# Performance work log

Hardware: AMD Instinct MI355X
Metric: run time of the kernel (lower is better)

The kernel has to match this reference:

```python
import jax, jax.numpy as jnp
import numpy as np

B, L, D = 4096, 200, 64
N_ITEMS, N_USERS, N_RATINGS = 100000, 100000, 5


def setup_inputs() -> dict:
    key = jax.random.key(0)
    ks = jax.random.split(key, 10)
    nodes = jax.random.randint(ks[0], (B,), 0, N_USERS)
    history_uv = jax.random.randint(ks[1], (B, L), 0, N_ITEMS)
    history_r = jax.random.randint(ks[2], (B, L), 0, N_RATINGS)
    s = 1.0 / np.sqrt(D)
    v2e = jax.random.normal(ks[3], (N_ITEMS, D), dtype=jnp.float32)
    r2e = jax.random.normal(ks[4], (N_RATINGS, D), dtype=jnp.float32)
    # torch Linear: weight is [out, in]
    w1_W = jax.random.uniform(ks[5], (D, 2 * D), dtype=jnp.float32, minval=-s, maxval=s)
    w1_b = jax.random.uniform(ks[6], (D,), dtype=jnp.float32, minval=-s, maxval=s)
    w2_W = jax.random.uniform(ks[7], (D, D), dtype=jnp.float32, minval=-s, maxval=s)
    w2_b = jax.random.uniform(ks[8], (D,), dtype=jnp.float32, minval=-s, maxval=s)
    return {
        "v2e": v2e, "r2e": r2e,
        "w1_W": w1_W, "w1_b": w1_b, "w2_W": w2_W, "w2_b": w2_b,
        "nodes": nodes, "history_uv": history_uv, "history_r": history_r,
    }


def reference(v2e, r2e, w1_W, w1_b, w2_W, w2_b, nodes, history_uv, history_r):
    # Gather item and rating embeddings for every (node, history slot): [B, L, D]
    e_uv = v2e[history_uv]
    e_r = r2e[history_r]
    # concat -> [B, L, 2D], two-layer MLP with ReLU
    x = jnp.concatenate([e_uv, e_r], axis=-1)
    h = jax.nn.relu(jnp.einsum("bli,oi->blo", x, w1_W) + w1_b)
    o = jax.nn.relu(jnp.einsum("bli,oi->blo", h, w2_W) + w2_b)
    # uv=True branch: plain mean over the history dimension (nodes/u2e unused)
    return jnp.mean(o, axis=1)  # [B, D]
```

## Files before the change

kernel.cpp:

```cpp
#include <hip/hip_runtime.h>

#define NITEMS 100000
#define NRATE  5
#define BB     4096
#define LL     200
#define DD     64
#define NTILES 6250
#define NWAVES 3128
#define NW_REM 3122

typedef short short8  __attribute__((ext_vector_type(8)));
typedef float f32x4   __attribute__((ext_vector_type(4)));
typedef float f32x2   __attribute__((ext_vector_type(2)));
typedef int   i32x4   __attribute__((ext_vector_type(4)));

static __device__ __forceinline__ short f2bf(float f) {
  return (short)((__builtin_bit_cast(unsigned, f) + 0x8000u) >> 16);
}
static __device__ __forceinline__ unsigned pk2bf(float a, float b) {
  const unsigned ua = __builtin_bit_cast(unsigned, a) + 0x8000u;
  const unsigned ub = __builtin_bit_cast(unsigned, b) + 0x8000u;
  return __builtin_amdgcn_perm(ub, ua, 0x07060302u);
}
static __device__ __forceinline__ int kperm(int p) {
  return ((p & 3) << 4) | (p >> 2);
}

#if __has_builtin(__builtin_elementwise_max)
static __device__ __forceinline__ f32x2 relu2(f32x2 v) {
  return __builtin_elementwise_max(v, f32x2{0.f, 0.f});
}
static __device__ __forceinline__ f32x4 relu4(f32x4 v) {
  return __builtin_elementwise_max(v, f32x4{0.f, 0.f, 0.f, 0.f});
}
#else
static __device__ __forceinline__ f32x2 relu2(f32x2 v) {
  return f32x2{fmaxf(v.x, 0.f), fmaxf(v.y, 0.f)};
}
static __device__ __forceinline__ f32x4 relu4(f32x4 v) {
  return f32x4{fmaxf(v[0], 0.f), fmaxf(v[1], 0.f), fmaxf(v[2], 0.f), fmaxf(v[3], 0.f)};
}
#endif

__global__ __launch_bounds__(256) void k_pre(
    const float* __restrict__ v2e, const float* __restrict__ r2e,
    const float* __restrict__ w1W, const float* __restrict__ w1b,
    const float* __restrict__ w2W,
    unsigned char* __restrict__ pre8, short* __restrict__ w2p,
    float* __restrict__ r5p)
{
  const int tid = threadIdx.x;
  const int blk = blockIdx.x;

  if (blk == 0) {
    for (int idx = tid; idx < 64 * 64; idx += 256) {
      const int o = idx >> 6, p = idx & 63;
      w2p[idx] = f2bf(w2W[o * 64 + kperm(p)]);
    }
    for (int idx = tid; idx < NRATE * 64; idx += 256) {
      const int r = idx >> 6, p = idx & 63;
      const int o = kperm(p);
      const float4* wr = reinterpret_cast<const float4*>(w1W + o * 128 + 64);
      const float4* rr = reinterpret_cast<const float4*>(r2e + r * 64);
      float s = w1b[o];
#pragma unroll
      for (int q = 0; q < 16; ++q) {
        const float4 a = wr[q], b = rr[q];
        s += a.x * b.x + a.y * b.y + a.z * b.z + a.w * b.w;
      }
      r5p[r * 64 + p] = s;
    }
    return;
  }

  const int wave = tid >> 6, lane = tid & 63;
  const int n = lane & 15, quad = lane >> 4;
  const int gw = (blk - 1) * 4 + wave;
  const int ntile = (gw < NW_REM) ? 2 : 1;

  const int q0 = ((n >> 1) & 3) * 16 + (n >> 3) * 8 + (n & 1) * 4;

  int tile = gw;
  float4 cur0, cur1, cur2, cur3;
  {
    const size_t row = (size_t)(tile * 16 + n);
    const float4* p = reinterpret_cast<const float4*>(v2e + row * 64 + quad * 8);
    cur0 = p[0]; cur1 = p[1];
    const float4* q = reinterpret_cast<const float4*>(v2e + row * 64 + 32 + quad * 8);
    cur2 = q[0]; cur3 = q[1];
  }

  short8 bfr[2][4];
#pragma unroll
  for (int nt = 0; nt < 4; ++nt)
#pragma unroll
    for (int kh = 0; kh < 2; ++kh) {
      const float4* p = reinterpret_cast<const float4*>(
          w1W + (nt * 16 + n) * 128 + kh * 32 + quad * 8);
      const float4 x0 = p[0], x1 = p[1];
      i32x4 pk = {(int)pk2bf(x0.x, x0.y), (int)pk2bf(x0.z, x0.w),
                  (int)pk2bf(x1.x, x1.y), (int)pk2bf(x1.z, x1.w)};
      bfr[kh][nt] = __builtin_bit_cast(short8, pk);
    }

  for (int it = 0; it < ntile; ++it) {
    const int next = tile + NWAVES;
    float4 nx0, nx1, nx2, nx3;
    if (it + 1 < ntile) {
      const size_t row = (size_t)(next * 16 + n);
      const float4* p = reinterpret_cast<const float4*>(v2e + row * 64 + quad * 8);
      nx0 = p[0]; nx1 = p[1];
      const float4* q = reinterpret_cast<const float4*>(v2e + row * 64 + 32 + quad * 8);
      nx2 = q[0]; nx3 = q[1];
    }

    short8 afr[2];
    {
      i32x4 pk0 = {(int)pk2bf(cur0.x, cur0.y), (int)pk2bf(cur0.z, cur0.w),
                   (int)pk2bf(cur1.x, cur1.y), (int)pk2bf(cur1.z, cur1.w)};
      afr[0] = __builtin_bit_cast(short8, pk0);
      i32x4 pk1 = {(int)pk2bf(cur2.x, cur2.y), (int)pk2bf(cur2.z, cur2.w),
                   (int)pk2bf(cur3.x, cur3.y), (int)pk2bf(cur3.z, cur3.w)};
      afr[1] = __builtin_bit_cast(short8, pk1);
    }

    f32x4 d[4];
#pragma unroll
    for (int nt = 0; nt < 4; ++nt) {
      f32x4 z = {0.f, 0.f, 0.f, 0.f};
      z = __builtin_amdgcn_mfma_f32_16x16x32_bf16(afr[0], bfr[0][nt], z, 0, 0, 0);
      z = __builtin_amdgcn_mfma_f32_16x16x32_bf16(afr[1], bfr[1][nt], z, 0, 0, 0);
      d[nt] = z;
    }

    const int ib = tile * 16;
#pragma unroll
    for (int r = 0; r < 4; ++r) {
      const int item = ib + quad * 4 + r;
      int pkd = 0;
      pkd = __builtin_amdgcn_cvt_pk_fp8_f32(d[0][r], d[1][r], pkd, false);
      pkd = __builtin_amdgcn_cvt_pk_fp8_f32(d[2][r], d[3][r], pkd, true);
      *reinterpret_cast<int*>(pre8 + (size_t)item * 64 + q0) = pkd;
    }

    tile = next;
    cur0 = nx0; cur1 = nx1; cur2 = nx2; cur3 = nx3;
  }
}

__global__ __launch_bounds__(256) void k_main(
    const unsigned char* __restrict__ pre8, const float* __restrict__ r5p,
    const short* __restrict__ w2p, const float* __restrict__ w2b,
    const int* __restrict__ huv, const int* __restrict__ hrr,
    float* __restrict__ out)
{
  __shared__ __align__(16) float s_r5[4][5 * 68];

  const int tid  = threadIdx.x;
  const int wave = tid >> 6, lane = tid & 63;
  const int n = lane & 15, quad = lane >> 4;
  const int b = blockIdx.x * 4 + wave;

  const int* hu = huv + b * LL;
  const int* hr = hrr + b * LL;

  int iv[13], ir[13];
#pragma unroll
  for (int t = 0; t < 12; ++t) {
    iv[t] = hu[t * 16 + n];
    ir[t] = hr[t * 16 + n];
  }
  {
    const int lc = min(192 + n, LL - 1);
    iv[12] = hu[lc];
    ir[12] = hr[lc];
  }

  i32x4 g[13];
#pragma unroll
  for (int t = 0; t < 13; ++t)
    g[t] = *reinterpret_cast<const i32x4*>(
        pre8 + (size_t)iv[t] * 64 + quad * 16);

#pragma unroll
  for (int i = 0; i < 5; ++i) {
    const int idx = i * 64 + lane;
    s_r5[wave][(idx >> 6) * 68 + (idx & 63)] = r5p[idx];
  }

  short8 bfr[2][4];
#pragma unroll
  for (int nt = 0; nt < 4; ++nt)
#pragma unroll
    for (int kh = 0; kh < 2; ++kh)
      bfr[kh][nt] = *reinterpret_cast<const short8*>(
          w2p + (nt * 16 + n) * 64 + kh * 32 + quad * 8);

  f32x4 zb[4];
#pragma unroll
  for (int nt = 0; nt < 4; ++nt) {
    const float bv = w2b[nt * 16 + n];
    zb[nt] = f32x4{bv, bv, bv, bv};
  }

  const float tailm = (quad < 2) ? 1.0f : 0.0f;
  f32x4 acc4[4] = {{0.f,0.f,0.f,0.f},{0.f,0.f,0.f,0.f},
                   {0.f,0.f,0.f,0.f},{0.f,0.f,0.f,0.f}};

#pragma unroll
  for (int t = 0; t < 13; ++t) {
    const float* rbase = &s_r5[wave][ir[t] * 68 + quad * 8];
    const f32x4 ra = *reinterpret_cast<const f32x4*>(rbase);
    const f32x4 rb = *reinterpret_cast<const f32x4*>(rbase + 4);
    const f32x4 rc = *reinterpret_cast<const f32x4*>(rbase + 32);
    const f32x4 rd = *reinterpret_cast<const f32x4*>(rbase + 36);

    short8 afr[2];
    {
      f32x2 p0 = relu2(__builtin_amdgcn_cvt_pk_f32_fp8(g[t][0], false) + f32x2{ra[0], ra[1]});
      f32x2 p1 = relu2(__builtin_amdgcn_cvt_pk_f32_fp8(g[t][0], true)  + f32x2{ra[2], ra[3]});
      f32x2 p2 = relu2(__builtin_amdgcn_cvt_pk_f32_fp8(g[t][1], false) + f32x2{rb[0], rb[1]});
      f32x2 p3 = relu2(__builtin_amdgcn_cvt_pk_f32_fp8(g[t][1], true)  + f32x2{rb[2], rb[3]});
      i32x4 hpk = {(int)pk2bf(p0.x, p0.y), (int)pk2bf(p1.x, p1.y),
                   (int)pk2bf(p2.x, p2.y), (int)pk2bf(p3.x, p3.y)};
      afr[0] = __builtin_bit_cast(short8, hpk);
    }
    {
      f32x2 p0 = relu2(__builtin_amdgcn_cvt_pk_f32_fp8(g[t][2], false) + f32x2{rc[0], rc[1]});
      f32x2 p1 = relu2(__builtin_amdgcn_cvt_pk_f32_fp8(g[t][2], true)  + f32x2{rc[2], rc[3]});
      f32x2 p2 = relu2(__builtin_amdgcn_cvt_pk_f32_fp8(g[t][3], false) + f32x2{rd[0], rd[1]});
      f32x2 p3 = relu2(__builtin_amdgcn_cvt_pk_f32_fp8(g[t][3], true)  + f32x2{rd[2], rd[3]});
      i32x4 hpk = {(int)pk2bf(p0.x, p0.y), (int)pk2bf(p1.x, p1.y),
                   (int)pk2bf(p2.x, p2.y), (int)pk2bf(p3.x, p3.y)};
      afr[1] = __builtin_bit_cast(short8, hpk);
    }

    __builtin_amdgcn_s_setprio(1);
    f32x4 d[4];
#pragma unroll
    for (int nt = 0; nt < 4; ++nt) {
      f32x4 z = zb[nt];
      z = __builtin_amdgcn_mfma_f32_16x16x32_bf16(afr[0], bfr[0][nt], z, 0, 0, 0);
      z = __builtin_amdgcn_mfma_f32_16x16x32_bf16(afr[1], bfr[1][nt], z, 0, 0, 0);
      d[nt] = z;
    }
    __builtin_amdgcn_s_setprio(0);

#pragma unroll
    for (int nt = 0; nt < 4; ++nt) {
      f32x4 mx = relu4(d[nt]);
      if (t == 12) mx = mx * tailm;
      acc4[nt] += mx;
    }
  }

  float acc[4];
#pragma unroll
  for (int nt = 0; nt < 4; ++nt) {
    float v = (acc4[nt][0] + acc4[nt][1]) + (acc4[nt][2] + acc4[nt][3]);
    v += __shfl_xor(v, 16, 64);
    v += __shfl_xor(v, 32, 64);
    acc[nt] = v;
  }

  out[b * 64 + quad * 16 + n] = acc[quad] * (1.0f / (float)LL);
}

__global__ __launch_bounds__(256) void k_fallback(
    const float* __restrict__ v2e, const float* __restrict__ r2e,
    const float* __restrict__ w1W, const float* __restrict__ w1b,
    const float* __restrict__ w2W, const float* __restrict__ w2b,
    const int* __restrict__ huv, const int* __restrict__ hrr,
    float* __restrict__ out)
{
  __shared__ float sw1[64][129];
  __shared__ float sw2[64][65];
  __shared__ float sx[4][128];
  __shared__ float sh[4][64];
  __shared__ float red[4][64];

  const int tid = threadIdx.x;
  const int wave = tid >> 6, lane = tid & 63;
  const int b = blockIdx.x;

  for (int idx = tid; idx < 64 * 128; idx += 256) sw1[idx >> 7][idx & 127] = w1W[idx];
  for (int idx = tid; idx < 64 * 64; idx += 256) sw2[idx >> 6][idx & 63] = w2W[idx];
  __syncthreads();

  const float b1o = w1b[lane], b2o = w2b[lane];
  float acc = 0.f;

  for (int l = wave; l < LL; l += 4) {
    const int iv = huv[b * LL + l];
    const int ir = hrr[b * LL + l];
    sx[wave][lane]      = v2e[iv * 64 + lane];
    sx[wave][64 + lane] = r2e[ir * 64 + lane];
    __syncthreads();
    float h = b1o;
    for (int i = 0; i < 128; ++i) h += sx[wave][i] * sw1[lane][i];
    sh[wave][lane] = fmaxf(h, 0.f);
    __syncthreads();
    float o = b2o;
    for (int i = 0; i < 64; ++i) o += sh[wave][i] * sw2[lane][i];
    acc += fmaxf(o, 0.f);
  }

  red[wave][lane] = acc;
  __syncthreads();
  if (tid < 64) {
    const float s = red[0][tid] + red[1][tid] + red[2][tid] + red[3][tid];
    out[b * 64 + tid] = s * (1.0f / (float)LL);
  }
}

extern "C" void kernel_launch(void* const* d_in, const int* in_sizes, int n_in,
                              void* d_out, int out_size, void* d_ws, size_t ws_size,
                              hipStream_t stream) {
  (void)in_sizes; (void)n_in; (void)out_size;
  const float* v2e = (const float*)d_in[0];
  const float* r2e = (const float*)d_in[1];
  const float* w1W = (const float*)d_in[2];
  const float* w1b = (const float*)d_in[3];
  const float* w2W = (const float*)d_in[4];
  const float* w2b = (const float*)d_in[5];
  const int* huv = (const int*)d_in[7];
  const int* hrr = (const int*)d_in[8];
  float* out = (float*)d_out;

  const size_t OFF_R5 = (size_t)NITEMS * 64;
  const size_t OFF_W2 = OFF_R5 + NRATE * 64 * sizeof(float);
  const size_t NEED   = OFF_W2 + 64 * 64 * sizeof(short);

  if (ws_size >= NEED) {
    unsigned char* pre8 = (unsigned char*)d_ws;
    float* r5p = (float*)((char*)d_ws + OFF_R5);
    short* w2p = (short*)((char*)d_ws + OFF_W2);

    k_pre<<<783, 256, 0, stream>>>(v2e, r2e, w1W, w1b, w2W, pre8, w2p, r5p);
    k_main<<<BB / 4, 256, 0, stream>>>(pre8, r5p, w2p, w2b, huv, hrr, out);
  } else {
    k_fallback<<<BB, 256, 0, stream>>>(v2e, r2e, w1W, w1b, w2W, w2b, huv, hrr, out);
  }
}
```

Baseline: 114.1 us.

## Process two batch rows per wave with all gathers issued up front

Each wave now handles two batch rows (b and b+2048). All 26 fp8 embedding-row gathers for both rows are issued before any compute, and the grid is halved to 512 blocks. Rating indices are packed into bytes, four per register, to offset the extra registers needed for the second row's gathered data. The aim is more memory-level parallelism per wave and amortised setup (W2 fragments, bias, rating table). The cost is higher register pressure, which can lower occupancy, and fewer waves overall.

```diff
diff --git a/kernel.cpp b/kernel.cpp
--- a/kernel.cpp
+++ b/kernel.cpp
@@ -148,68 +148,19 @@
   }
 }
 
-__global__ __launch_bounds__(256) void k_main(
-    const unsigned char* __restrict__ pre8, const float* __restrict__ r5p,
-    const short* __restrict__ w2p, const float* __restrict__ w2b,
-    const int* __restrict__ huv, const int* __restrict__ hrr,
-    float* __restrict__ out)
+static __device__ __forceinline__ void tiles_b(
+    const i32x4 (&g)[13], const unsigned (&irp)[4],
+    const float* r5w, const short8 (&bfr)[2][4], const f32x4 (&zb)[4],
+    const int n, const int quad, const float tailm,
+    float* __restrict__ out, const int b)
 {
-  __shared__ __align__(16) float s_r5[4][5 * 68];
-
-  const int tid  = threadIdx.x;
-  const int wave = tid >> 6, lane = tid & 63;
-  const int n = lane & 15, quad = lane >> 4;
-  const int b = blockIdx.x * 4 + wave;
-
-  const int* hu = huv + b * LL;
-  const int* hr = hrr + b * LL;
-
-  int iv[13], ir[13];
-#pragma unroll
-  for (int t = 0; t < 12; ++t) {
-    iv[t] = hu[t * 16 + n];
-    ir[t] = hr[t * 16 + n];
-  }
-  {
-    const int lc = min(192 + n, LL - 1);
-    iv[12] = hu[lc];
-    ir[12] = hr[lc];
-  }
-
-  i32x4 g[13];
-#pragma unroll
-  for (int t = 0; t < 13; ++t)
-    g[t] = *reinterpret_cast<const i32x4*>(
-        pre8 + (size_t)iv[t] * 64 + quad * 16);
-
-#pragma unroll
-  for (int i = 0; i < 5; ++i) {
-    const int idx = i * 64 + lane;
-    s_r5[wave][(idx >> 6) * 68 + (idx & 63)] = r5p[idx];
-  }
-
-  short8 bfr[2][4];
-#pragma unroll
-  for (int nt = 0; nt < 4; ++nt)
-#pragma unroll
-    for (int kh = 0; kh < 2; ++kh)
-      bfr[kh][nt] = *reinterpret_cast<const short8*>(
-          w2p + (nt * 16 + n) * 64 + kh * 32 + quad * 8);
-
-  f32x4 zb[4];
-#pragma unroll
-  for (int nt = 0; nt < 4; ++nt) {
-    const float bv = w2b[nt * 16 + n];
-    zb[nt] = f32x4{bv, bv, bv, bv};
-  }
-
-  const float tailm = (quad < 2) ? 1.0f : 0.0f;
   f32x4 acc4[4] = {{0.f,0.f,0.f,0.f},{0.f,0.f,0.f,0.f},
                    {0.f,0.f,0.f,0.f},{0.f,0.f,0.f,0.f}};
 
 #pragma unroll
   for (int t = 0; t < 13; ++t) {
-    const float* rbase = &s_r5[wave][ir[t] * 68 + quad * 8];
+    const int irt = (int)((irp[t >> 2] >> ((t & 3) * 8)) & 0xFF);
+    const float* rbase = r5w + irt * 68 + quad * 8;
     const f32x4 ra = *reinterpret_cast<const f32x4*>(rbase);
     const f32x4 rb = *reinterpret_cast<const f32x4*>(rbase + 4);
     const f32x4 rc = *reinterpret_cast<const f32x4*>(rbase + 32);
@@ -262,8 +213,84 @@
     v += __shfl_xor(v, 32, 64);
     acc[nt] = v;
   }
-
   out[b * 64 + quad * 16 + n] = acc[quad] * (1.0f / (float)LL);
+}
+
+__global__ __launch_bounds__(256) void k_main(
+    const unsigned char* __restrict__ pre8, const float* __restrict__ r5p,
+    const short* __restrict__ w2p, const float* __restrict__ w2b,
+    const int* __restrict__ huv, const int* __restrict__ hrr,
+    float* __restrict__ out)
+{
+  __shared__ __align__(16) float s_r5[4][5 * 68];
+
+  const int tid  = threadIdx.x;
+  const int wave = tid >> 6, lane = tid & 63;
+  const int n = lane & 15, quad = lane >> 4;
+  const int gw = blockIdx.x * 4 + wave;
+  const int b1 = gw, b2 = gw + 2048;
+
+  int iv1[13], iv2[13];
+  unsigned irp1[4] = {0u,0u,0u,0u}, irp2[4] = {0u,0u,0u,0u};
+  {
+    const int* hu = huv + b1 * LL; const int* hr = hrr + b1 * LL;
+#pragma unroll
+    for (int t = 0; t < 12; ++t) {
+      iv1[t] = hu[t * 16 + n];
+      irp1[t >> 2] |= ((unsigned)hr[t * 16 + n]) << ((t & 3) * 8);
+    }
+    const int lc = min(192 + n, LL - 1);
+    iv1[12] = hu[lc];
+    irp1[3] |= (unsigned)hr[lc];
+  }
+  {
+    const int* hu = huv + b2 * LL; const int* hr = hrr + b2 * LL;
+#pragma unroll
+    for (int t = 0; t < 12; ++t) {
+      iv2[t] = hu[t * 16 + n];
+      irp2[t >> 2] |= ((unsigned)hr[t * 16 + n]) << ((t & 3) * 8);
+    }
+    const int lc = min(192 + n, LL - 1);
+    iv2[12] = hu[lc];
+    irp2[3] |= (unsigned)hr[lc];
+  }
+
+  i32x4 g1[13], g2[13];
+#pragma unroll
+  for (int t = 0; t < 13; ++t)
+    g1[t] = *reinterpret_cast<const i32x4*>(
+        pre8 + (size_t)iv1[t] * 64 + quad * 16);
+#pragma unroll
+  for (int t = 0; t < 13; ++t)
+    g2[t] = *reinterpret_cast<const i32x4*>(
+        pre8 + (size_t)iv2[t] * 64 + quad * 16);
+
+#pragma unroll
+  for (int i = 0; i < 5; ++i) {
+    const int idx = i * 64 + lane;
+    s_r5[wave][(idx >> 6) * 68 + (idx & 63)] = r5p[idx];
+  }
+
+  short8 bfr[2][4];
+#pragma unroll
+  for (int nt = 0; nt < 4; ++nt)
+#pragma unroll
+    for (int kh = 0; kh < 2; ++kh)
+      bfr[kh][nt] = *reinterpret_cast<const short8*>(
+          w2p + (nt * 16 + n) * 64 + kh * 32 + quad * 8);
+
+  f32x4 zb[4];
+#pragma unroll
+  for (int nt = 0; nt < 4; ++nt) {
+    const float bv = w2b[nt * 16 + n];
+    zb[nt] = f32x4{bv, bv, bv, bv};
+  }
+
+  const float tailm = (quad < 2) ? 1.0f : 0.0f;
+  const float* r5w = &s_r5[wave][0];
+
+  tiles_b(g1, irp1, r5w, bfr, zb, n, quad, tailm, out, b1);
+  tiles_b(g2, irp2, r5w, bfr, zb, n, quad, tailm, out, b2);
 }
 
 __global__ __launch_bounds__(256) void k_fallback(
@@ -337,7 +364,7 @@
     short* w2p = (short*)((char*)d_ws + OFF_W2);
 
     k_pre<<<783, 256, 0, stream>>>(v2e, r2e, w1W, w1b, w2W, pre8, w2p, r5p);
-    k_main<<<BB / 4, 256, 0, stream>>>(pre8, r5p, w2p, w2b, huv, hrr, out);
+    k_main<<<512, 256, 0, stream>>>(pre8, r5p, w2p, w2b, huv, hrr, out);
   } else {
     k_fallback<<<BB, 256, 0, stream>>>(v2e, r2e, w1W, w1b, w2W, w2b, huv, hrr, out);
   }
```

Measured after the change: 119.0 us. +4.3%, slower.
